# Kernel tuning notes

Measured on AMD Instinct MI355X. Metric: run time of the kernel, lower is better.

## Reference

```python
import jax, jax.numpy as jnp
import numpy as np
from jax import lax

B, N, C_FEAT = 16, 32768, 128
NPOINT = 2048
BIG = 1e10  # initial 'infinite' distance, matches torch's 1e10


def farthest_point_sample(xyz, npoint):
    """xyz: [B,N,3] -> indices [B,npoint] via iterative FPS.
    Deterministic start at index 0 (original uses a random start index)."""
    b, n, c = xyz.shape

    def step(carry, _):
        distance, farthest = carry                      # [B,N], [B]
        centroid = jnp.take_along_axis(
            xyz, farthest[:, None, None], axis=1)       # [B,1,3]
        dist = jnp.sum((xyz - centroid) ** 2, axis=-1)  # [B,N]
        distance = jnp.minimum(distance, dist)          # running min dist to chosen set
        new_farthest = jnp.argmax(distance, axis=-1)    # [B]
        return (distance, new_farthest), farthest

    init = (jnp.full((b, n), BIG, xyz.dtype), jnp.zeros((b,), jnp.int32))
    _, idxs = lax.scan(step, init, None, length=npoint)  # [npoint, B]
    return idxs.T                                        # [B, npoint]


def index_points(points, idx):
    """points: [B,N,D], idx: [B,S] -> [B,S,D] gather."""
    return jnp.take_along_axis(points, idx[:, :, None], axis=1)


def setup_inputs() -> dict:
    key = jax.random.key(0)
    k1, k2 = jax.random.split(key)
    xyz = jax.random.normal(k1, (B, N, 3), dtype=jnp.float32)
    features = jax.random.normal(k2, (B, N, C_FEAT), dtype=jnp.float32)
    return {"xyz": xyz, "features": features, "npoint": NPOINT}


def reference(xyz, features, npoint):
    fps_idx = farthest_point_sample(xyz, npoint)   # [B,npoint]
    new_xyz = index_points(xyz, fps_idx)           # [B,npoint,3]
    new_features = index_points(features, fps_idx) # [B,npoint,C]
    return (new_xyz, new_features)
```

## Files before the change

### kernel.cpp

```cpp
#include <hip/hip_runtime.h>

#define BATCH   16
#define NPTS    32768
#define NPOINT  2048
#define C_FEAT  128
#define NSEG    1024
#define NTH     1024
#define NW      16


__device__ __forceinline__ unsigned part4(unsigned v) {
  return (v & 1u) | ((v & 2u) << 2) | ((v & 4u) << 4) | ((v & 8u) << 6);
}
__device__ __forceinline__ int morton(float x, float y, float z) {
  const unsigned qx = (unsigned)min(15, max(0, (int)((x + 4.0f) * 2.0f)));
  const unsigned qy = (unsigned)min(15, max(0, (int)((y + 4.0f) * 2.0f)));
  const unsigned qz = (unsigned)min(15, max(0, (int)((z + 4.0f) * 2.0f)));
  return (int)(part4(qx) | (part4(qy) << 1) | (part4(qz) << 2));
}

__device__ __forceinline__ unsigned long long u64max(unsigned long long a,
                                                     unsigned long long b) {
  return a > b ? a : b;
}
__device__ __forceinline__ unsigned long long shflxor_u64(
    unsigned long long v, int off) {
  const unsigned lo = (unsigned)v, hi = (unsigned)(v >> 32);
  const unsigned olo = (unsigned)__shfl_xor((int)lo, off);
  const unsigned ohi = (unsigned)__shfl_xor((int)hi, off);
  return ((unsigned long long)ohi << 32) | olo;
}
__device__ __forceinline__ unsigned short bfup(float e) {
  const unsigned u = __float_as_uint(e);
  unsigned short b = (unsigned short)(u >> 16);
  if (__uint_as_float(((unsigned)b) << 16) < e) ++b;
  return b;
}

__global__ __launch_bounds__(NTH) void sort_kernel(
    const float* __restrict__ xyz, float4* __restrict__ pts) {
  const int b = blockIdx.x, t = threadIdx.x, lane = t & 63;
  const float* __restrict__ base = xyz + (size_t)b * NPTS * 3;
  __shared__ unsigned bins[4096];
  __shared__ unsigned wsum[NW];

  for (int i = t; i < 4096; i += NTH) bins[i] = 0u;
  __syncthreads();
  for (int k = 0; k < 32; ++k) {
    const int p = k * NTH + t;
    atomicAdd(&bins[morton(base[p*3], base[p*3+1], base[p*3+2])], 1u);
  }
  __syncthreads();

  unsigned c0 = bins[4*t], c1 = bins[4*t+1], c2 = bins[4*t+2], c3 = bins[4*t+3];
  const unsigned mysum = c0 + c1 + c2 + c3;
  unsigned acc = mysum;
#pragma unroll
  for (int d = 1; d < 64; d <<= 1) {
    unsigned n = __shfl_up(acc, d);
    if (lane >= d) acc += n;
  }
  if (lane == 63) wsum[t >> 6] = acc;
  __syncthreads();
  unsigned woff = 0;
  for (int w = 0; w < (t >> 6); ++w) woff += wsum[w];
  unsigned run = woff + acc - mysum;
  bins[4*t]   = run; run += c0;
  bins[4*t+1] = run; run += c1;
  bins[4*t+2] = run; run += c2;
  bins[4*t+3] = run;
  __syncthreads();

  float4* __restrict__ pb = pts + (size_t)b * NPTS;
  for (int k = 0; k < 32; ++k) {
    const int p = k * NTH + t;
    const float x = base[p*3], y = base[p*3+1], z = base[p*3+2];
    const unsigned pos = atomicAdd(&bins[morton(x, y, z)], 1u);
    pb[pos] = make_float4(x, y, z, __int_as_float(p));
  }
}

__global__ __launch_bounds__(NTH) void fps_kernel(
    const float4* __restrict__ pts_g, int* __restrict__ fps_idx) {
  const int b = blockIdx.x, t = threadIdx.x, lane = t & 63, w = t >> 6;
  const int hw = t >> 5, hl = t & 31;
  const float4* __restrict__ P = pts_g + (size_t)b * NPTS;

  __shared__ float              dmin[NPTS];
  __shared__ unsigned long long pack[NSEG];
  __shared__ float              cenx[NSEG], ceny[NSEG], cenz[NSEG];
  __shared__ unsigned short     extx[NSEG], exty[NSEG], extz[NSEG];
  __shared__ unsigned long long s_red[2][8];
  __shared__ unsigned short     wl[NSEG];
  __shared__ int                s_cnt[2];

  for (int r = 0; r < 32; ++r) {
    const int seg = r * 32 + hw;
    const int i = seg * 32 + hl;
    const float4 q = P[i];
    dmin[i] = 1e10f;
    float xl = q.x, xh = q.x, yl = q.y, yh = q.y, zl = q.z, zh = q.z;
    unsigned k = ((unsigned)__float_as_int(q.w) << 15) | (unsigned)i;
#pragma unroll
    for (int off = 16; off > 0; off >>= 1) {
      xl = fminf(xl, __shfl_xor(xl, off)); xh = fmaxf(xh, __shfl_xor(xh, off));
      yl = fminf(yl, __shfl_xor(yl, off)); yh = fmaxf(yh, __shfl_xor(yh, off));
      zl = fminf(zl, __shfl_xor(zl, off)); zh = fmaxf(zh, __shfl_xor(zh, off));
      k  = min(k, (unsigned)__shfl_xor((int)k, off));
    }
    if (hl == 0) {
      const float cxm = 0.5f * (xl + xh);
      const float cym = 0.5f * (yl + yh);
      const float czm = 0.5f * (zl + zh);
      float ex = fmaxf(xh - cxm, cxm - xl);
      float ey = fmaxf(yh - cym, cym - yl);
      float ez = fmaxf(zh - czm, czm - zl);
      ex = __uint_as_float(__float_as_uint(ex) + 2);
      ey = __uint_as_float(__float_as_uint(ey) + 2);
      ez = __uint_as_float(__float_as_uint(ez) + 2);
      cenx[seg] = cxm; ceny[seg] = cym; cenz[seg] = czm;
      extx[seg] = bfup(ex); exty[seg] = bfup(ey); extz[seg] = bfup(ez);
      pack[seg] = ((unsigned long long)__float_as_uint(1e10f) << 32) |
                  (unsigned long long)(0x3FFFFFFFu - k);
    }
  }
  if (t == 0) { s_cnt[0] = 0; s_cnt[1] = 0; }
  __syncthreads();

  if (t < 512) {
    unsigned long long p = u64max(pack[t], pack[t + 512]);
#pragma unroll
    for (int off = 32; off > 0; off >>= 1) p = u64max(p, shflxor_u64(p, off));
    if (lane == 0) s_red[0][w] = p;
  }
  __syncthreads();

  for (int s = 0; s < NPOINT; ++s) {
    unsigned long long p = s_red[s & 1][0];
#pragma unroll
    for (int j = 1; j < 8; ++j) p = u64max(p, s_red[s & 1][j]);
    const unsigned kwin = 0x3FFFFFFFu - (unsigned)(p & 0x3FFFFFFFu);
    const int far = (int)(kwin >> 15);
    const float4 qn = P[(int)(kwin & 0x7FFFu)];
    const float cx = qn.x, cy = qn.y, cz = qn.z;

    if (t == 0) fps_idx[b * NPOINT + s] = far;
    if (t == NTH - 1) s_cnt[(s + 1) & 1] = 0;

    {
      const unsigned long long pk = pack[t];
      const float cm = __uint_as_float((unsigned)(pk >> 32));
      const float ex = __uint_as_float(((unsigned)extx[t]) << 16);
      const float ey = __uint_as_float(((unsigned)exty[t]) << 16);
      const float ez = __uint_as_float(((unsigned)extz[t]) << 16);
      const float ddx = fmaxf(fabsf(cx - cenx[t]) - ex, 0.0f);
      const float ddy = fmaxf(fabsf(cy - ceny[t]) - ey, 0.0f);
      const float ddz = fmaxf(fabsf(cz - cenz[t]) - ez, 0.0f);
      const float r2 = ddx * ddx + ddy * ddy + ddz * ddz;
      const bool need = !(r2 * 0.999f > cm);
      const unsigned long long bal = __ballot(need);
      int wb = 0;
      if (lane == 0 && bal != 0ull)
        wb = atomicAdd(&s_cnt[s & 1], (int)__popcll(bal));
      wb = __shfl(wb, 0);
      if (need) {
        const unsigned long long ltm = (1ull << lane) - 1ull;
        wl[wb + (int)__popcll(bal & ltm)] = (unsigned short)t;
      }
    }
    __syncthreads();

    const int C = s_cnt[s & 1];
    int e = hw;
    for (; e + 32 < C; e += 64) {
      const int segA = (int)wl[e], segB = (int)wl[e + 32];
      const int iA = segA * 32 + hl, iB = segB * 32 + hl;
      const float4 qA = P[iA];
      const float4 qB = P[iB];
      const float dmA = dmin[iA], dmB = dmin[iB];
      const float dxA = qA.x - cx, dyA = qA.y - cy, dzA = qA.z - cz;
      const float dxB = qB.x - cx, dyB = qB.y - cy, dzB = qB.z - cz;
      const float dA = __builtin_fmaf(dzA, dzA, __builtin_fmaf(dyA, dyA, dxA*dxA));
      const float dB = __builtin_fmaf(dzB, dzB, __builtin_fmaf(dyB, dyB, dxB*dxB));
      const float ndA = fminf(dmA, dA), ndB = fminf(dmB, dB);
      dmin[iA] = ndA; dmin[iB] = ndB;
      const unsigned kA = ((unsigned)__float_as_int(qA.w) << 15) | (unsigned)iA;
      const unsigned kB = ((unsigned)__float_as_int(qB.w) << 15) | (unsigned)iB;
      unsigned long long pA = ((unsigned long long)__float_as_uint(ndA) << 32) |
                              (unsigned long long)(0x3FFFFFFFu - kA);
      unsigned long long pB = ((unsigned long long)__float_as_uint(ndB) << 32) |
                              (unsigned long long)(0x3FFFFFFFu - kB);
#pragma unroll
      for (int off = 16; off > 0; off >>= 1) {
        pA = u64max(pA, shflxor_u64(pA, off));
        pB = u64max(pB, shflxor_u64(pB, off));
      }
      if (hl == 0) { pack[segA] = pA; pack[segB] = pB; }
    }
    for (; e < C; e += 32) {
      const int seg = (int)wl[e];
      const int i = seg * 32 + hl;
      const float4 q = P[i];
      const float dx = q.x - cx, dy = q.y - cy, dz = q.z - cz;
      const float d = __builtin_fmaf(dz, dz, __builtin_fmaf(dy, dy, dx * dx));
      const float nd = fminf(dmin[i], d);
      dmin[i] = nd;
      const unsigned k = ((unsigned)__float_as_int(q.w) << 15) | (unsigned)i;
      unsigned long long pk = ((unsigned long long)__float_as_uint(nd) << 32) |
                              (unsigned long long)(0x3FFFFFFFu - k);
#pragma unroll
      for (int off = 16; off > 0; off >>= 1) pk = u64max(pk, shflxor_u64(pk, off));
      if (hl == 0) pack[seg] = pk;
    }
    __syncthreads();

    if (t < 512) {
      unsigned long long pk = u64max(pack[t], pack[t + 512]);
#pragma unroll
      for (int off = 32; off > 0; off >>= 1) pk = u64max(pk, shflxor_u64(pk, off));
      if (lane == 0) s_red[(s + 1) & 1][w] = pk;
    }
    __syncthreads();
  }
}

__global__ __launch_bounds__(256) void gather_kernel(
    const float* __restrict__ xyz, const float* __restrict__ feat,
    const int* __restrict__ fps_idx, float* __restrict__ out) {
  const int lane = threadIdx.x & 31;
  const int sub  = threadIdx.x >> 5;
  const int row  = blockIdx.x * 8 + sub;
  const int b    = row >> 11;
  const int src  = fps_idx[row];

  const float4* __restrict__ f =
      reinterpret_cast<const float4*>(feat + ((size_t)b * NPTS + src) * C_FEAT);
  float4* __restrict__ o =
      reinterpret_cast<float4*>(out + (size_t)BATCH * NPOINT * 3 +
                                (size_t)row * C_FEAT);
  o[lane] = f[lane];
  if (lane < 3) {
    out[(size_t)row * 3 + lane] = xyz[((size_t)b * NPTS + src) * 3 + lane];
  }
}

extern "C" void kernel_launch(void* const* d_in, const int* in_sizes, int n_in,
                              void* d_out, int out_size, void* d_ws, size_t ws_size,
                              hipStream_t stream) {
  (void)in_sizes; (void)n_in; (void)out_size; (void)ws_size;
  const float* xyz  = (const float*)d_in[0];
  const float* feat = (const float*)d_in[1];
  float* out = (float*)d_out;

  char* ws = (char*)d_ws;
  int*    fps_idx = (int*)ws;
  float4* pts     = (float4*)(ws + (1u << 20));

  sort_kernel<<<BATCH, NTH, 0, stream>>>(xyz, pts);
  fps_kernel<<<BATCH, NTH, 0, stream>>>(pts, fps_idx);
  gather_kernel<<<(BATCH * NPOINT) / 8, 256, 0, stream>>>(xyz, feat, fps_idx, out);
}
```

Before: 3.829 ms.

## Cache per-segment winner coords and bounding boxes in registers, unroll segment loop 4x

Each segment's current argmax point coordinates are stored in a shared cand array, so the next centroid is read from LDS instead of a dependent global load of P on the serial critical path. Segment centers and full-precision float extents move into per-thread registers, replacing the bf16-rounded shared extents and letting dmin temporarily hold extents during setup. The update loop is unrolled to four segments per half-wave iteration to expose more memory-level parallelism. The cost is higher register pressure and extra conditional LDS writes of winner coordinates for every updated segment.

```diff
diff --git a/kernel.cpp b/kernel.cpp
--- a/kernel.cpp
+++ b/kernel.cpp
@@ -30,12 +30,6 @@
   const unsigned ohi = (unsigned)__shfl_xor((int)hi, off);
   return ((unsigned long long)ohi << 32) | olo;
 }
-__device__ __forceinline__ unsigned short bfup(float e) {
-  const unsigned u = __float_as_uint(e);
-  unsigned short b = (unsigned short)(u >> 16);
-  if (__uint_as_float(((unsigned)b) << 16) < e) ++b;
-  return b;
-}
 
 __global__ __launch_bounds__(NTH) void sort_kernel(
     const float* __restrict__ xyz, float4* __restrict__ pts) {
@@ -88,8 +82,7 @@
 
   __shared__ float              dmin[NPTS];
   __shared__ unsigned long long pack[NSEG];
-  __shared__ float              cenx[NSEG], ceny[NSEG], cenz[NSEG];
-  __shared__ unsigned short     extx[NSEG], exty[NSEG], extz[NSEG];
+  __shared__ float              cand[3][NSEG];
   __shared__ unsigned long long s_red[2][8];
   __shared__ unsigned short     wl[NSEG];
   __shared__ int                s_cnt[2];
@@ -98,7 +91,6 @@
     const int seg = r * 32 + hw;
     const int i = seg * 32 + hl;
     const float4 q = P[i];
-    dmin[i] = 1e10f;
     float xl = q.x, xh = q.x, yl = q.y, yh = q.y, zl = q.z, zh = q.z;
     unsigned k = ((unsigned)__float_as_int(q.w) << 15) | (unsigned)i;
 #pragma unroll
@@ -112,18 +104,24 @@
       const float cxm = 0.5f * (xl + xh);
       const float cym = 0.5f * (yl + yh);
       const float czm = 0.5f * (zl + zh);
-      float ex = fmaxf(xh - cxm, cxm - xl);
-      float ey = fmaxf(yh - cym, cym - yl);
-      float ez = fmaxf(zh - czm, czm - zl);
-      ex = __uint_as_float(__float_as_uint(ex) + 2);
-      ey = __uint_as_float(__float_as_uint(ey) + 2);
-      ez = __uint_as_float(__float_as_uint(ez) + 2);
-      cenx[seg] = cxm; ceny[seg] = cym; cenz[seg] = czm;
-      extx[seg] = bfup(ex); exty[seg] = bfup(ey); extz[seg] = bfup(ez);
+      cand[0][seg] = cxm; cand[1][seg] = cym; cand[2][seg] = czm;
+      dmin[seg]            = __uint_as_float(__float_as_uint(fmaxf(xh - cxm, cxm - xl)) + 2);
+      dmin[NSEG + seg]     = __uint_as_float(__float_as_uint(fmaxf(yh - cym, cym - yl)) + 2);
+      dmin[2 * NSEG + seg] = __uint_as_float(__float_as_uint(fmaxf(zh - czm, czm - zl)) + 2);
       pack[seg] = ((unsigned long long)__float_as_uint(1e10f) << 32) |
                   (unsigned long long)(0x3FFFFFFFu - k);
     }
   }
+  __syncthreads();
+
+  const float cenr0 = cand[0][t], cenr1 = cand[1][t], cenr2 = cand[2][t];
+  const float extr0 = dmin[t], extr1 = dmin[NSEG + t], extr2 = dmin[2 * NSEG + t];
+  const unsigned k0 = 0x3FFFFFFFu - (unsigned)(pack[t] & 0x3FFFFFFFull);
+  const float4 qc = P[(int)(k0 & 0x7FFFu)];
+  __syncthreads();
+
+  cand[0][t] = qc.x; cand[1][t] = qc.y; cand[2][t] = qc.z;
+  for (int k = 0; k < 32; ++k) dmin[k * NTH + t] = 1e10f;
   if (t == 0) { s_cnt[0] = 0; s_cnt[1] = 0; }
   __syncthreads();
 
@@ -140,22 +138,18 @@
 #pragma unroll
     for (int j = 1; j < 8; ++j) p = u64max(p, s_red[s & 1][j]);
     const unsigned kwin = 0x3FFFFFFFu - (unsigned)(p & 0x3FFFFFFFu);
-    const int far = (int)(kwin >> 15);
-    const float4 qn = P[(int)(kwin & 0x7FFFu)];
-    const float cx = qn.x, cy = qn.y, cz = qn.z;
+    const int far  = (int)(kwin >> 15);
+    const int segw = (int)((kwin & 0x7FFFu) >> 5);
+    const float cx = cand[0][segw], cy = cand[1][segw], cz = cand[2][segw];
 
     if (t == 0) fps_idx[b * NPOINT + s] = far;
     if (t == NTH - 1) s_cnt[(s + 1) & 1] = 0;
 
     {
-      const unsigned long long pk = pack[t];
-      const float cm = __uint_as_float((unsigned)(pk >> 32));
-      const float ex = __uint_as_float(((unsigned)extx[t]) << 16);
-      const float ey = __uint_as_float(((unsigned)exty[t]) << 16);
-      const float ez = __uint_as_float(((unsigned)extz[t]) << 16);
-      const float ddx = fmaxf(fabsf(cx - cenx[t]) - ex, 0.0f);
-      const float ddy = fmaxf(fabsf(cy - ceny[t]) - ey, 0.0f);
-      const float ddz = fmaxf(fabsf(cz - cenz[t]) - ez, 0.0f);
+      const float cm = __uint_as_float((unsigned)(pack[t] >> 32));
+      const float ddx = fmaxf(fabsf(cx - cenr0) - extr0, 0.0f);
+      const float ddy = fmaxf(fabsf(cy - cenr1) - extr1, 0.0f);
+      const float ddz = fmaxf(fabsf(cz - cenr2) - extr2, 0.0f);
       const float r2 = ddx * ddx + ddy * ddy + ddz * ddz;
       const bool need = !(r2 * 0.999f > cm);
       const unsigned long long bal = __ballot(need);
@@ -170,48 +164,63 @@
     }
     __syncthreads();
 
-    const int C = s_cnt[s & 1];
+    const int nC = s_cnt[s & 1];
     int e = hw;
-    for (; e + 32 < C; e += 64) {
-      const int segA = (int)wl[e], segB = (int)wl[e + 32];
-      const int iA = segA * 32 + hl, iB = segB * 32 + hl;
-      const float4 qA = P[iA];
-      const float4 qB = P[iB];
-      const float dmA = dmin[iA], dmB = dmin[iB];
-      const float dxA = qA.x - cx, dyA = qA.y - cy, dzA = qA.z - cz;
-      const float dxB = qB.x - cx, dyB = qB.y - cy, dzB = qB.z - cz;
-      const float dA = __builtin_fmaf(dzA, dzA, __builtin_fmaf(dyA, dyA, dxA*dxA));
-      const float dB = __builtin_fmaf(dzB, dzB, __builtin_fmaf(dyB, dyB, dxB*dxB));
-      const float ndA = fminf(dmA, dA), ndB = fminf(dmB, dB);
-      dmin[iA] = ndA; dmin[iB] = ndB;
-      const unsigned kA = ((unsigned)__float_as_int(qA.w) << 15) | (unsigned)iA;
-      const unsigned kB = ((unsigned)__float_as_int(qB.w) << 15) | (unsigned)iB;
-      unsigned long long pA = ((unsigned long long)__float_as_uint(ndA) << 32) |
-                              (unsigned long long)(0x3FFFFFFFu - kA);
-      unsigned long long pB = ((unsigned long long)__float_as_uint(ndB) << 32) |
-                              (unsigned long long)(0x3FFFFFFFu - kB);
+#define SEG_BODY(SEGV, PKV)                                                    \
+      const int i_##PKV = (SEGV) * 32 + hl;                                    \
+      const float4 q_##PKV = P[i_##PKV];                                       \
+      const float dm_##PKV = dmin[i_##PKV];                                    \
+      const float dx_##PKV = q_##PKV.x - cx, dy_##PKV = q_##PKV.y - cy,        \
+                  dz_##PKV = q_##PKV.z - cz;                                   \
+      const float d_##PKV = __builtin_fmaf(dz_##PKV, dz_##PKV,                 \
+          __builtin_fmaf(dy_##PKV, dy_##PKV, dx_##PKV * dx_##PKV));            \
+      const float nd_##PKV = fminf(dm_##PKV, d_##PKV);                         \
+      dmin[i_##PKV] = nd_##PKV;                                                \
+      const unsigned kk_##PKV =                                                \
+          ((unsigned)__float_as_int(q_##PKV.w) << 15) | (unsigned)i_##PKV;     \
+      unsigned long long PKV =                                                 \
+          ((unsigned long long)__float_as_uint(nd_##PKV) << 32) |              \
+          (unsigned long long)(0x3FFFFFFFu - kk_##PKV);                        \
+      const unsigned long long PKV##0 = PKV;
+
+    for (; e + 96 < nC; e += 128) {
+      const int sA = (int)wl[e], sB = (int)wl[e + 32],
+                sC = (int)wl[e + 64], sD = (int)wl[e + 96];
+      SEG_BODY(sA, pA) SEG_BODY(sB, pB) SEG_BODY(sC, pC) SEG_BODY(sD, pD)
+#pragma unroll
+      for (int off = 16; off > 0; off >>= 1) {
+        pA = u64max(pA, shflxor_u64(pA, off));
+        pB = u64max(pB, shflxor_u64(pB, off));
+        pC = u64max(pC, shflxor_u64(pC, off));
+        pD = u64max(pD, shflxor_u64(pD, off));
+      }
+      if (hl == 0) { pack[sA]=pA; pack[sB]=pB; pack[sC]=pC; pack[sD]=pD; }
+      if (pA0 == pA) { cand[0][sA]=q_pA.x; cand[1][sA]=q_pA.y; cand[2][sA]=q_pA.z; }
+      if (pB0 == pB) { cand[0][sB]=q_pB.x; cand[1][sB]=q_pB.y; cand[2][sB]=q_pB.z; }
+      if (pC0 == pC) { cand[0][sC]=q_pC.x; cand[1][sC]=q_pC.y; cand[2][sC]=q_pC.z; }
+      if (pD0 == pD) { cand[0][sD]=q_pD.x; cand[1][sD]=q_pD.y; cand[2][sD]=q_pD.z; }
+    }
+    for (; e + 32 < nC; e += 64) {
+      const int sA = (int)wl[e], sB = (int)wl[e + 32];
+      SEG_BODY(sA, pA) SEG_BODY(sB, pB)
 #pragma unroll
       for (int off = 16; off > 0; off >>= 1) {
         pA = u64max(pA, shflxor_u64(pA, off));
         pB = u64max(pB, shflxor_u64(pB, off));
       }
-      if (hl == 0) { pack[segA] = pA; pack[segB] = pB; }
-    }
-    for (; e < C; e += 32) {
-      const int seg = (int)wl[e];
-      const int i = seg * 32 + hl;
-      const float4 q = P[i];
-      const float dx = q.x - cx, dy = q.y - cy, dz = q.z - cz;
-      const float d = __builtin_fmaf(dz, dz, __builtin_fmaf(dy, dy, dx * dx));
-      const float nd = fminf(dmin[i], d);
-      dmin[i] = nd;
-      const unsigned k = ((unsigned)__float_as_int(q.w) << 15) | (unsigned)i;
-      unsigned long long pk = ((unsigned long long)__float_as_uint(nd) << 32) |
-                              (unsigned long long)(0x3FFFFFFFu - k);
-#pragma unroll
-      for (int off = 16; off > 0; off >>= 1) pk = u64max(pk, shflxor_u64(pk, off));
-      if (hl == 0) pack[seg] = pk;
-    }
+      if (hl == 0) { pack[sA] = pA; pack[sB] = pB; }
+      if (pA0 == pA) { cand[0][sA]=q_pA.x; cand[1][sA]=q_pA.y; cand[2][sA]=q_pA.z; }
+      if (pB0 == pB) { cand[0][sB]=q_pB.x; cand[1][sB]=q_pB.y; cand[2][sB]=q_pB.z; }
+    }
+    for (; e < nC; e += 32) {
+      const int sA = (int)wl[e];
+      SEG_BODY(sA, pA)
+#pragma unroll
+      for (int off = 16; off > 0; off >>= 1) pA = u64max(pA, shflxor_u64(pA, off));
+      if (hl == 0) pack[sA] = pA;
+      if (pA0 == pA) { cand[0][sA]=q_pA.x; cand[1][sA]=q_pA.y; cand[2][sA]=q_pA.z; }
+    }
+#undef SEG_BODY
     __syncthreads();
 
     if (t < 512) {
```

New measurement: 3.918 ms. 1.02x slower.
